# Kernel tuning notes

Measured on AMD Instinct MI355X. Metric: run time of the kernel, lower is better.

Reference implementation:

```python
import jax, jax.numpy as jnp
import numpy as np

N_NODES = 100000
N_EDGES = 1600000
IN_FEATS = 128
OUT_FEATS = 64


def setup_inputs() -> dict:
    key = jax.random.key(0)
    k1, k2, k3, k4 = jax.random.split(key, 4)
    feat = jax.random.normal(k1, (N_NODES, IN_FEATS), dtype=jnp.float32)
    W = jax.random.normal(k2, (IN_FEATS, OUT_FEATS), dtype=jnp.float32) * (1.0 / np.sqrt(IN_FEATS))
    src = jax.random.randint(k3, (N_EDGES,), 0, N_NODES, dtype=jnp.int64)
    dst = jax.random.randint(k4, (N_EDGES,), 0, N_NODES, dtype=jnp.int64)
    return {"feat": feat, "W": W, "src": src, "dst": dst}


def reference(feat, W, src, dst):
    # Linear projection (bias=False): homogeneous graph -> shared fc
    ft = feat @ W  # [N, out]

    # per-edge dot-product score: e_ij = <ft[src], ft[dst]>
    a = jnp.sum(ft[src] * ft[dst], axis=-1)  # [E]

    # edge softmax segmented by destination node (numerically stable)
    neg_inf = jnp.finfo(a.dtype).min
    m = jax.ops.segment_max(a, dst, num_segments=N_NODES)  # [N]
    m = jnp.where(m == neg_inf, 0.0, m)  # guard zero-in-degree nodes
    e = jnp.exp(a - m[dst])  # [E]
    s = jax.ops.segment_sum(e, dst, num_segments=N_NODES)  # [N]
    s = jnp.where(s == 0.0, 1.0, s)
    sa = e / s[dst]  # [E]

    # weighted scatter-sum aggregation: out[i] = sum_{j in N(i)} sa_ij * ft[j]
    rst = jax.ops.segment_sum(ft[src] * sa[:, None], dst, num_segments=N_NODES)
    return rst
```

## Files before the change

kernel.cpp:

```cpp
#include <hip/hip_runtime.h>
#include <hip/hip_fp16.h>
#include <math.h>

#define N_NODES 100000
#define N_EDGES 1600000
#define IN_F    128
#define OUT_F   64
#define NQ        782
#define Q_SHIFT   7
#define Q_NODES   128
#define QCAP      3072
#define CHUNK     4096
#define PBLKS     ((N_EDGES + CHUNK - 1) / CHUNK)
#define LTILES    (N_NODES / 16)
#define LBLKS     ((LTILES + 3) / 4)

typedef _Float16 half8 __attribute__((ext_vector_type(8)));
typedef _Float16 h2 __attribute__((ext_vector_type(2)));
typedef _Float16 h4 __attribute__((ext_vector_type(4)));
typedef __fp16   q2v __attribute__((ext_vector_type(2)));
typedef float    f32x4 __attribute__((ext_vector_type(4)));

__device__ __forceinline__ float fdot2f(h2 a, h2 b, float c) {
#if __has_builtin(__builtin_amdgcn_fdot2)
    return __builtin_amdgcn_fdot2(__builtin_bit_cast(q2v, a), __builtin_bit_cast(q2v, b), c, false);
#else
    return (float)a[0] * (float)b[0] + (float)a[1] * (float)b[1] + c;
#endif
}

#if __has_builtin(__builtin_amdgcn_update_dpp)
#define DPP_ADD(x, ctrl)                                                                  \
    (x) += __builtin_bit_cast(float, __builtin_amdgcn_update_dpp(                         \
               0, __builtin_bit_cast(int, (x)), (ctrl), 0xF, 0xF, true))
#define REDUCE16(x) do { DPP_ADD(x, 0xB1); DPP_ADD(x, 0x4E); \
                         DPP_ADD(x, 0x141); DPP_ADD(x, 0x140); } while (0)
#else
#define REDUCE16(x) do { x += __shfl_xor(x, 1); x += __shfl_xor(x, 2); \
                         x += __shfl_xor(x, 4); x += __shfl_xor(x, 8); } while (0)
#endif


__global__ __launch_bounds__(256) void partition_linear_kernel(const int* __restrict__ src,
                                                               const int* __restrict__ dst,
                                                               unsigned* __restrict__ staging,
                                                               int* __restrict__ pcnt,
                                                               int* __restrict__ pbase,
                                                               const float* __restrict__ feat,
                                                               const float* __restrict__ W,
                                                               __half* __restrict__ fth) {
    __shared__ int hist[1024], lbase[1024], sc[256];
    __shared__ unsigned sval[CHUNK];
    int t = threadIdx.x;
    if (blockIdx.x < PBLKS) {
        hist[t] = 0; hist[t + 256] = 0; hist[t + 512] = 0; hist[t + 768] = 0;
        __syncthreads();
        int beg = blockIdx.x * CHUNK;
        int end = min(beg + CHUNK, N_EDGES);
        for (int i = beg + t; i < end; i += 256)
            atomicAdd(&hist[dst[i] >> Q_SHIFT], 1);
        __syncthreads();
        int h0 = hist[4 * t], h1 = hist[4 * t + 1], h2i = hist[4 * t + 2], h3 = hist[4 * t + 3];
        int tot = h0 + h1 + h2i + h3;
        sc[t] = tot;
        __syncthreads();
        for (int off = 1; off < 256; off <<= 1) {
            int add = (t >= off) ? sc[t - off] : 0;
            __syncthreads();
            sc[t] += add;
            __syncthreads();
        }
        int excl = sc[t] - tot;
        int b0 = excl, b1 = excl + h0, b2 = b1 + h1, b3 = b2 + h2i;
        lbase[4 * t] = b0; lbase[4 * t + 1] = b1; lbase[4 * t + 2] = b2; lbase[4 * t + 3] = b3;
        *(int4*)(pcnt  + (size_t)blockIdx.x * 1024 + 4 * t) = make_int4(h0, h1, h2i, h3);
        *(int4*)(pbase + (size_t)blockIdx.x * 1024 + 4 * t) = make_int4(b0, b1, b2, b3);
        hist[4 * t] = 0; hist[4 * t + 1] = 0; hist[4 * t + 2] = 0; hist[4 * t + 3] = 0;
        __syncthreads();
        for (int i = beg + t; i < end; i += 256) {
            int s = src[i], d = dst[i];
            int b = d >> Q_SHIFT;
            int r = atomicAdd(&hist[b], 1);
            sval[lbase[b] + r] = (unsigned)s | ((unsigned)(d & (Q_NODES - 1)) << 17);
        }
        __syncthreads();
        int n = end - beg;
        for (int p = t; p < n; p += 256)
            staging[(size_t)blockIdx.x * CHUNK + p] = sval[p];
        return;
    }
    int gwave = (blockIdx.x - PBLKS) * 4 + (t >> 6);
    if (gwave >= LTILES) return;
    int lane = t & 63;
    int m = lane & 15, kg = lane >> 4;
    int r0 = gwave * 16;

    half8 fb[4][4];
#pragma unroll
    for (int kb = 0; kb < 4; ++kb)
#pragma unroll
        for (int nb = 0; nb < 4; ++nb) {
            const float* wp = W + (size_t)(kb * 32 + kg * 8) * OUT_F + nb * 16 + m;
#pragma unroll
            for (int j = 0; j < 8; ++j)
                fb[kb][nb][j] = (_Float16)wp[j * OUT_F];
        }

    f32x4 acc[4];
#pragma unroll
    for (int nb = 0; nb < 4; ++nb) acc[nb] = (f32x4){0.f, 0.f, 0.f, 0.f};

#pragma unroll
    for (int kb = 0; kb < 4; ++kb) {
        const float4* ap = (const float4*)(feat + (size_t)(r0 + m) * IN_F + kb * 32 + kg * 8);
        float4 a0 = ap[0], a1 = ap[1];
        half8 fa = {(_Float16)a0.x, (_Float16)a0.y, (_Float16)a0.z, (_Float16)a0.w,
                    (_Float16)a1.x, (_Float16)a1.y, (_Float16)a1.z, (_Float16)a1.w};
#pragma unroll
        for (int nb = 0; nb < 4; ++nb)
            acc[nb] = __builtin_amdgcn_mfma_f32_16x16x32_f16(fa, fb[kb][nb], acc[nb], 0, 0, 0);
    }
#pragma unroll
    for (int nb = 0; nb < 4; ++nb)
#pragma unroll
        for (int i = 0; i < 4; ++i)
            fth[(size_t)(r0 + kg * 4 + i) * OUT_F + nb * 16 + m] = __float2half_rn(acc[nb][i]);
}

__global__ __launch_bounds__(1024) void quarter_fused_kernel(const unsigned* __restrict__ staging,
                                                             const int* __restrict__ pcnt,
                                                             const int* __restrict__ pbase,
                                                             const __half* __restrict__ fth,
                                                             float* __restrict__ out) {
    const float LOG2E = 1.44269504088896340736f;
    __shared__ unsigned sbuf[QCAP];
    __shared__ int csr[QCAP];
    __shared__ int exo[PBLKS], pbs[PBLKS], scnt[PBLKS];
    __shared__ int s512[512];
    __shared__ int cnt[Q_NODES], rbeg[Q_NODES], lcur[Q_NODES];
    __shared__ int ntot;
    int t = threadIdx.x;
    int qq = blockIdx.x;

    int d = 0;
    if (t < PBLKS) { d = pcnt[(size_t)t * 1024 + qq]; pbs[t] = pbase[(size_t)t * 1024 + qq]; scnt[t] = d; }
    if (t < 512) s512[t] = (t < PBLKS) ? d : 0;
    if (t < Q_NODES) cnt[t] = 0;
    __syncthreads();
    for (int off = 1; off < 512; off <<= 1) {
        int add = (t >= off && t < 512) ? s512[t - off] : 0;
        __syncthreads();
        if (t < 512) s512[t] += add;
        __syncthreads();
    }
    if (t < PBLKS) exo[t] = s512[t] - d;
    if (t == PBLKS - 1) ntot = s512[t];
    __syncthreads();
    int n = ntot;

    {
        int wid = t >> 6, ln = t & 63;
        int sg0 = wid * 8 + (ln >> 3), j0 = ln & 7;
        for (int s = sg0; s < PBLKS; s += 128) {
            int c = scnt[s], eo = exo[s];
            size_t gb = (size_t)s * CHUNK + pbs[s];
            for (int j = j0; j < c; j += 8)
                sbuf[eo + j] = staging[gb + j];
        }
    }
    __syncthreads();

    for (int i = t; i < n; i += 1024)
        atomicAdd(&cnt[sbuf[i] >> 17], 1);
    __syncthreads();
    if (t < Q_NODES) s512[t] = cnt[t];
    __syncthreads();
    for (int off = 1; off < Q_NODES; off <<= 1) {
        int add = (t >= off && t < Q_NODES) ? s512[t - off] : 0;
        __syncthreads();
        if (t < Q_NODES) s512[t] += add;
        __syncthreads();
    }
    if (t < Q_NODES) { int v = cnt[t]; int b0 = s512[t] - v; rbeg[t] = b0; lcur[t] = b0; }
    __syncthreads();
    for (int i = t; i < n; i += 1024) {
        unsigned u = sbuf[i];
        int pos = atomicAdd(&lcur[u >> 17], 1);
        csr[pos] = (int)(u & 0x1FFFFu);
    }
    __syncthreads();

    int wid = t >> 6, lane = t & 63;
    int q = lane >> 4, ql = lane & 15;
    const _Float16* fh = (const _Float16*)fth;
#pragma unroll
    for (int k = 0; k < 8; ++k) {
        int ln = wid + 16 * k;
        int node = qq * Q_NODES + ln;
        int beg = rbeg[ln];
        int end = beg + cnt[ln];

        h4 rdv = (node < N_NODES)
                   ? *(const h4*)(fh + (size_t)node * OUT_F + 4 * ql) : (h4){0, 0, 0, 0};
        h2 dlo = __builtin_shufflevector(rdv, rdv, 0, 1);
        h2 dhi = __builtin_shufflevector(rdv, rdv, 2, 3);

        float m = -1e30f, l = 0.f;
        float a0 = 0.f, a1 = 0.f, a2 = 0.f, a3 = 0.f;

        for (int i = beg; i < end; i += 16) {
            int e0 = i + q, e1 = e0 + 4, e2 = e0 + 8, e3 = e0 + 12;
            bool u0 = e0 < end, u1 = e1 < end, u2 = e2 < end, u3 = e3 < end;
            int s0 = csr[u0 ? e0 : beg];
            int s1 = csr[u1 ? e1 : beg];
            int s2 = csr[u2 ? e2 : beg];
            int s3 = csr[u3 ? e3 : beg];
            h4 rA = *(const h4*)(fh + (size_t)s0 * OUT_F + 4 * ql);
            h4 rB = *(const h4*)(fh + (size_t)s1 * OUT_F + 4 * ql);
            h4 rC = *(const h4*)(fh + (size_t)s2 * OUT_F + 4 * ql);
            h4 rD = *(const h4*)(fh + (size_t)s3 * OUT_F + 4 * ql);

            float p0 = fdot2f(__builtin_shufflevector(rA, rA, 0, 1), dlo,
                       fdot2f(__builtin_shufflevector(rA, rA, 2, 3), dhi, 0.f));
            float p1 = fdot2f(__builtin_shufflevector(rB, rB, 0, 1), dlo,
                       fdot2f(__builtin_shufflevector(rB, rB, 2, 3), dhi, 0.f));
            float p2 = fdot2f(__builtin_shufflevector(rC, rC, 0, 1), dlo,
                       fdot2f(__builtin_shufflevector(rC, rC, 2, 3), dhi, 0.f));
            float p3 = fdot2f(__builtin_shufflevector(rD, rD, 0, 1), dlo,
                       fdot2f(__builtin_shufflevector(rD, rD, 2, 3), dhi, 0.f));
            REDUCE16(p0);
            REDUCE16(p1);
            REDUCE16(p2);
            REDUCE16(p3);
            p0 = u0 ? p0 * LOG2E : -1e30f;
            p1 = u1 ? p1 * LOG2E : -1e30f;
            p2 = u2 ? p2 * LOG2E : -1e30f;
            p3 = u3 ? p3 * LOG2E : -1e30f;

            float nm = fmaxf(fmaxf(fmaxf(p0, p1), fmaxf(p2, p3)), m);
            float alpha = exp2f(m - nm);
            float w0 = exp2f(p0 - nm), w1 = exp2f(p1 - nm);
            float w2 = exp2f(p2 - nm), w3 = exp2f(p3 - nm);
            l = l * alpha + ((w0 + w1) + (w2 + w3));
#if __has_builtin(__builtin_amdgcn_cvt_pkrtz)
            h2 wlo = __builtin_bit_cast(h2, __builtin_amdgcn_cvt_pkrtz(w0, w1));
            h2 whi = __builtin_bit_cast(h2, __builtin_amdgcn_cvt_pkrtz(w2, w3));
#else
            h2 wlo = {(_Float16)w0, (_Float16)w1};
            h2 whi = {(_Float16)w2, (_Float16)w3};
#endif
            h2 cab0 = {rA[0], rB[0]}, ccd0 = {rC[0], rD[0]};
            h2 cab1 = {rA[1], rB[1]}, ccd1 = {rC[1], rD[1]};
            h2 cab2 = {rA[2], rB[2]}, ccd2 = {rC[2], rD[2]};
            h2 cab3 = {rA[3], rB[3]}, ccd3 = {rC[3], rD[3]};
            a0 = fdot2f(wlo, cab0, fdot2f(whi, ccd0, a0 * alpha));
            a1 = fdot2f(wlo, cab1, fdot2f(whi, ccd1, a1 * alpha));
            a2 = fdot2f(wlo, cab2, fdot2f(whi, ccd2, a2 * alpha));
            a3 = fdot2f(wlo, cab3, fdot2f(whi, ccd3, a3 * alpha));
            m = nm;
        }

#pragma unroll
        for (int dd = 16; dd <= 32; dd <<= 1) {
            float m2 = __shfl_xor(m, dd), l2 = __shfl_xor(l, dd);
            float b0 = __shfl_xor(a0, dd), b1 = __shfl_xor(a1, dd);
            float b2 = __shfl_xor(a2, dd), b3 = __shfl_xor(a3, dd);
            float M = fmaxf(m, m2);
            float e1 = exp2f(m - M), e2 = exp2f(m2 - M);
            l = l * e1 + l2 * e2;
            a0 = a0 * e1 + b0 * e2;
            a1 = a1 * e1 + b1 * e2;
            a2 = a2 * e1 + b2 * e2;
            a3 = a3 * e1 + b3 * e2;
            m = M;
        }
        if (q == 0 && node < N_NODES) {
            float inv = (l > 0.f) ? 1.f / l : 0.f;
            *(float4*)(out + (size_t)node * OUT_F + 4 * ql) =
                make_float4(a0 * inv, a1 * inv, a2 * inv, a3 * inv);
        }
    }
}

extern "C" void kernel_launch(void* const* d_in, const int* in_sizes, int n_in,
                              void* d_out, int out_size, void* d_ws, size_t ws_size,
                              hipStream_t stream) {
    const float* feat = (const float*)d_in[0];
    const float* W    = (const float*)d_in[1];
    const int*   src  = (const int*)d_in[2];
    const int*   dst  = (const int*)d_in[3];
    float* out = (float*)d_out;

    __half*   fth      = (__half*)d_ws;
    unsigned* staging  = (unsigned*)((int*)d_ws + (size_t)N_NODES * OUT_F / 2);
    int*      pcnt     = (int*)(staging + (size_t)PBLKS * CHUNK);
    int*      pbase    = pcnt + (size_t)PBLKS * 1024;

    partition_linear_kernel<<<PBLKS + LBLKS, 256, 0, stream>>>(src, dst, staging, pcnt, pbase,
                                                               feat, W, fth);
    quarter_fused_kernel<<<NQ, 1024, 0, stream>>>(staging, pcnt, pbase, fth, out);
}
```

Before: 188.4 us.

## Pack partition metadata, use wave-shuffle scans, fuse histogram, share softmax max

Packs the per-chunk count and base into one 32-bit word, which halves the metadata reads in the fused kernel. The block-wide LDS prefix scans, with their many __syncthreads, are replaced by single-wave shuffle scans. The per-node histogram is folded into the staging copy loop. The online softmax now shares its running max across the four quarter-lanes, so rescaling happens only when the max grows and the final merge becomes a plain sum. The risk is that the 16-bit packing limits counts and bases to CHUNK-sized values, and that the branch on a new max may diverge.

```diff
diff --git a/kernel.cpp b/kernel.cpp
--- a/kernel.cpp
+++ b/kernel.cpp
@@ -44,8 +44,7 @@
 __global__ __launch_bounds__(256) void partition_linear_kernel(const int* __restrict__ src,
                                                                const int* __restrict__ dst,
                                                                unsigned* __restrict__ staging,
-                                                               int* __restrict__ pcnt,
-                                                               int* __restrict__ pbase,
+                                                               unsigned* __restrict__ pmeta,
                                                                const float* __restrict__ feat,
                                                                const float* __restrict__ W,
                                                                __half* __restrict__ fth) {
@@ -73,8 +72,9 @@
         int excl = sc[t] - tot;
         int b0 = excl, b1 = excl + h0, b2 = b1 + h1, b3 = b2 + h2i;
         lbase[4 * t] = b0; lbase[4 * t + 1] = b1; lbase[4 * t + 2] = b2; lbase[4 * t + 3] = b3;
-        *(int4*)(pcnt  + (size_t)blockIdx.x * 1024 + 4 * t) = make_int4(h0, h1, h2i, h3);
-        *(int4*)(pbase + (size_t)blockIdx.x * 1024 + 4 * t) = make_int4(b0, b1, b2, b3);
+        *(uint4*)(pmeta + (size_t)blockIdx.x * 1024 + 4 * t) =
+            make_uint4(((unsigned)h0 << 16) | b0, ((unsigned)h1 << 16) | b1,
+                       ((unsigned)h2i << 16) | b2, ((unsigned)h3 << 16) | b3);
         hist[4 * t] = 0; hist[4 * t + 1] = 0; hist[4 * t + 2] = 0; hist[4 * t + 3] = 0;
         __syncthreads();
         for (int i = beg + t; i < end; i += 256) {
@@ -128,33 +128,45 @@
 }
 
 __global__ __launch_bounds__(1024) void quarter_fused_kernel(const unsigned* __restrict__ staging,
-                                                             const int* __restrict__ pcnt,
-                                                             const int* __restrict__ pbase,
+                                                             const unsigned* __restrict__ pmeta,
                                                              const __half* __restrict__ fth,
                                                              float* __restrict__ out) {
     const float LOG2E = 1.44269504088896340736f;
     __shared__ unsigned sbuf[QCAP];
     __shared__ int csr[QCAP];
-    __shared__ int exo[PBLKS], pbs[PBLKS], scnt[PBLKS];
-    __shared__ int s512[512];
+    __shared__ unsigned smeta[PBLKS];
+    __shared__ int exo[PBLKS];
     __shared__ int cnt[Q_NODES], rbeg[Q_NODES], lcur[Q_NODES];
     __shared__ int ntot;
     int t = threadIdx.x;
     int qq = blockIdx.x;
 
-    int d = 0;
-    if (t < PBLKS) { d = pcnt[(size_t)t * 1024 + qq]; pbs[t] = pbase[(size_t)t * 1024 + qq]; scnt[t] = d; }
-    if (t < 512) s512[t] = (t < PBLKS) ? d : 0;
+    if (t < PBLKS) smeta[t] = pmeta[(size_t)t * 1024 + qq];
     if (t < Q_NODES) cnt[t] = 0;
     __syncthreads();
-    for (int off = 1; off < 512; off <<= 1) {
-        int add = (t >= off && t < 512) ? s512[t - off] : 0;
-        __syncthreads();
-        if (t < 512) s512[t] += add;
-        __syncthreads();
-    }
-    if (t < PBLKS) exo[t] = s512[t] - d;
-    if (t == PBLKS - 1) ntot = s512[t];
+    if (t < 64) {
+        int s0 = t * 7;
+        int loc[7];
+        int sum = 0;
+#pragma unroll
+        for (int j = 0; j < 7; ++j) {
+            int s = s0 + j;
+            int v = (s < PBLKS) ? (int)(smeta[s] >> 16) : 0;
+            loc[j] = sum;
+            sum += v;
+        }
+        int inc = sum;
+#pragma unroll
+        for (int d = 1; d < 64; d <<= 1) {
+            int o = __shfl_up(inc, d);
+            if (t >= d) inc += o;
+        }
+        int excl = inc - sum;
+#pragma unroll
+        for (int j = 0; j < 7; ++j)
+            if (s0 + j < PBLKS) exo[s0 + j] = excl + loc[j];
+        if (t == 63) ntot = inc;
+    }
     __syncthreads();
     int n = ntot;
 
@@ -162,26 +174,32 @@
         int wid = t >> 6, ln = t & 63;
         int sg0 = wid * 8 + (ln >> 3), j0 = ln & 7;
         for (int s = sg0; s < PBLKS; s += 128) {
-            int c = scnt[s], eo = exo[s];
-            size_t gb = (size_t)s * CHUNK + pbs[s];
-            for (int j = j0; j < c; j += 8)
-                sbuf[eo + j] = staging[gb + j];
-        }
-    }
-    __syncthreads();
-
-    for (int i = t; i < n; i += 1024)
-        atomicAdd(&cnt[sbuf[i] >> 17], 1);
-    __syncthreads();
-    if (t < Q_NODES) s512[t] = cnt[t];
-    __syncthreads();
-    for (int off = 1; off < Q_NODES; off <<= 1) {
-        int add = (t >= off && t < Q_NODES) ? s512[t - off] : 0;
-        __syncthreads();
-        if (t < Q_NODES) s512[t] += add;
-        __syncthreads();
-    }
-    if (t < Q_NODES) { int v = cnt[t]; int b0 = s512[t] - v; rbeg[t] = b0; lcur[t] = b0; }
+            unsigned meta = smeta[s];
+            int c = (int)(meta >> 16), pb = (int)(meta & 0xFFFFu);
+            int eo = exo[s];
+            size_t gb = (size_t)s * CHUNK + pb;
+            for (int j = j0; j < c; j += 8) {
+                unsigned u = staging[gb + j];
+                sbuf[eo + j] = u;
+                atomicAdd(&cnt[u >> 17], 1);
+            }
+        }
+    }
+    __syncthreads();
+
+    if (t < 64) {
+        int c0 = cnt[2 * t], c1 = cnt[2 * t + 1];
+        int s = c0 + c1;
+        int inc = s;
+#pragma unroll
+        for (int d = 1; d < 64; d <<= 1) {
+            int o = __shfl_up(inc, d);
+            if (t >= d) inc += o;
+        }
+        int excl = inc - s;
+        rbeg[2 * t] = excl;     lcur[2 * t] = excl;
+        rbeg[2 * t + 1] = excl + c0; lcur[2 * t + 1] = excl + c0;
+    }
     __syncthreads();
     for (int i = t; i < n; i += 1024) {
         unsigned u = sbuf[i];
@@ -237,11 +255,18 @@
             p2 = u2 ? p2 * LOG2E : -1e30f;
             p3 = u3 ? p3 * LOG2E : -1e30f;
 
-            float nm = fmaxf(fmaxf(fmaxf(p0, p1), fmaxf(p2, p3)), m);
-            float alpha = exp2f(m - nm);
-            float w0 = exp2f(p0 - nm), w1 = exp2f(p1 - nm);
-            float w2 = exp2f(p2 - nm), w3 = exp2f(p3 - nm);
-            l = l * alpha + ((w0 + w1) + (w2 + w3));
+            float pm = fmaxf(fmaxf(p0, p1), fmaxf(p2, p3));
+            pm = fmaxf(pm, __shfl_xor(pm, 16));
+            pm = fmaxf(pm, __shfl_xor(pm, 32));
+            if (pm > m) {
+                float alpha = exp2f(m - pm);
+                l *= alpha;
+                a0 *= alpha; a1 *= alpha; a2 *= alpha; a3 *= alpha;
+                m = pm;
+            }
+            float w0 = exp2f(p0 - m), w1 = exp2f(p1 - m);
+            float w2 = exp2f(p2 - m), w3 = exp2f(p3 - m);
+            l += (w0 + w1) + (w2 + w3);
 #if __has_builtin(__builtin_amdgcn_cvt_pkrtz)
             h2 wlo = __builtin_bit_cast(h2, __builtin_amdgcn_cvt_pkrtz(w0, w1));
             h2 whi = __builtin_bit_cast(h2, __builtin_amdgcn_cvt_pkrtz(w2, w3));
@@ -253,26 +278,19 @@
             h2 cab1 = {rA[1], rB[1]}, ccd1 = {rC[1], rD[1]};
             h2 cab2 = {rA[2], rB[2]}, ccd2 = {rC[2], rD[2]};
             h2 cab3 = {rA[3], rB[3]}, ccd3 = {rC[3], rD[3]};
-            a0 = fdot2f(wlo, cab0, fdot2f(whi, ccd0, a0 * alpha));
-            a1 = fdot2f(wlo, cab1, fdot2f(whi, ccd1, a1 * alpha));
-            a2 = fdot2f(wlo, cab2, fdot2f(whi, ccd2, a2 * alpha));
-            a3 = fdot2f(wlo, cab3, fdot2f(whi, ccd3, a3 * alpha));
-            m = nm;
+            a0 = fdot2f(wlo, cab0, fdot2f(whi, ccd0, a0));
+            a1 = fdot2f(wlo, cab1, fdot2f(whi, ccd1, a1));
+            a2 = fdot2f(wlo, cab2, fdot2f(whi, ccd2, a2));
+            a3 = fdot2f(wlo, cab3, fdot2f(whi, ccd3, a3));
         }
 
 #pragma unroll
         for (int dd = 16; dd <= 32; dd <<= 1) {
-            float m2 = __shfl_xor(m, dd), l2 = __shfl_xor(l, dd);
-            float b0 = __shfl_xor(a0, dd), b1 = __shfl_xor(a1, dd);
-            float b2 = __shfl_xor(a2, dd), b3 = __shfl_xor(a3, dd);
-            float M = fmaxf(m, m2);
-            float e1 = exp2f(m - M), e2 = exp2f(m2 - M);
-            l = l * e1 + l2 * e2;
-            a0 = a0 * e1 + b0 * e2;
-            a1 = a1 * e1 + b1 * e2;
-            a2 = a2 * e1 + b2 * e2;
-            a3 = a3 * e1 + b3 * e2;
-            m = M;
+            l  += __shfl_xor(l, dd);
+            a0 += __shfl_xor(a0, dd);
+            a1 += __shfl_xor(a1, dd);
+            a2 += __shfl_xor(a2, dd);
+            a3 += __shfl_xor(a3, dd);
         }
         if (q == 0 && node < N_NODES) {
             float inv = (l > 0.f) ? 1.f / l : 0.f;
@@ -293,10 +311,9 @@
 
     __half*   fth      = (__half*)d_ws;
     unsigned* staging  = (unsigned*)((int*)d_ws + (size_t)N_NODES * OUT_F / 2);
-    int*      pcnt     = (int*)(staging + (size_t)PBLKS * CHUNK);
-    int*      pbase    = pcnt + (size_t)PBLKS * 1024;
-
-    partition_linear_kernel<<<PBLKS + LBLKS, 256, 0, stream>>>(src, dst, staging, pcnt, pbase,
+    unsigned* pmeta    = staging + (size_t)PBLKS * CHUNK;
+
+    partition_linear_kernel<<<PBLKS + LBLKS, 256, 0, stream>>>(src, dst, staging, pmeta,
                                                                feat, W, fth);
-    quarter_fused_kernel<<<NQ, 1024, 0, stream>>>(staging, pcnt, pbase, fth, out);
+    quarter_fused_kernel<<<NQ, 1024, 0, stream>>>(staging, pmeta, fth, out);
 }
```

New measurement: 178.6 us. -5.2%, faster.
